# Performance work log

Hardware: AMD Instinct MI355X
Metric: run time of the kernel (lower is better)

Reference implementation:

```python
import jax, jax.numpy as jnp
import numpy as np
from jax.scipy.special import gammaln

NSTEP, NGRID, MU, LENF = 730, 1500, 16, 15
PRECS = 1e-5

# [low, high] physical ranges for the 12 HBV parameters (same order as torch code)
PARA_SCALE = np.array([[1, 6], [50, 1000], [0.05, 0.9], [0.01, 0.5], [0.001, 0.2],
                       [0.2, 1], [0, 10], [0, 100], [-2.5, 2.5], [0.5, 10],
                       [0, 0.1], [0, 0.2]], dtype=np.float32)
ROUT_SCALE = np.array([[0, 2.9], [0, 6.5]], dtype=np.float32)


def setup_inputs() -> dict:
    key = jax.random.key(0)
    kp, kt, ke, kpar, krt = jax.random.split(key, 5)
    P = jax.random.uniform(kp, (NSTEP, NGRID), jnp.float32) * 10.0   # precip mm/day
    T = jax.random.normal(kt, (NSTEP, NGRID), jnp.float32) * 8.0     # temp degC
    ETp = jax.random.uniform(ke, (NSTEP, NGRID), jnp.float32) * 5.0  # PET mm/day
    x = jnp.stack([P, T, ETp], axis=-1)                              # [Nstep, Ngrid, 3]
    parameters = jax.random.uniform(kpar, (NGRID, 12, MU), jnp.float32)
    rtwts = jax.random.uniform(krt, (NGRID, 2), jnp.float32)
    return {"x": x, "parameters": parameters, "rtwts": rtwts, "mu": MU}


def _hbv(x, parameters, rtwts, mu):
    Nstep, Ngrid = x.shape[0], x.shape[1]
    # scale raw [0,1] parameters into physical ranges; each is [Ngrid, mu]
    lo, hi = PARA_SCALE[:, 0], PARA_SCALE[:, 1]
    par = [lo[i] + parameters[:, i, :] * (hi[i] - lo[i]) for i in range(12)]
    (parBETA, parFC, parK0, parK1, parK2, parLP, parPERC, parUZL,
     parTT, parCFMAX, parCFR, parCWH) = par

    P, T, ETp = x[:, :, 0], x[:, :, 1], x[:, :, 2]  # each [Nstep, Ngrid]

    init = tuple(jnp.full((Ngrid, mu), 0.001, jnp.float32) for _ in range(5))

    def step(carry, inp):
        SNOWPACK, MELTWATER, SM, SUZ, SLZ = carry
        Pt, Tt, Et = inp
        Pm, Tm, ETpm = Pt[:, None], Tt[:, None], Et[:, None]  # [Ngrid, 1]
        is_rain = (Tm >= parTT).astype(jnp.float32)
        RAIN = Pm * is_rain
        SNOW = Pm * (1.0 - is_rain)
        SNOWPACK = SNOWPACK + SNOW
        melt = jnp.minimum(jnp.maximum(parCFMAX * (Tm - parTT), 0.0), SNOWPACK)
        MELTWATER = MELTWATER + melt
        SNOWPACK = SNOWPACK - melt
        refreezing = jnp.minimum(jnp.maximum(parCFR * parCFMAX * (parTT - Tm), 0.0), MELTWATER)
        SNOWPACK = SNOWPACK + refreezing
        MELTWATER = MELTWATER - refreezing
        tosoil = jnp.maximum(MELTWATER - parCWH * SNOWPACK, 0.0)
        MELTWATER = MELTWATER - tosoil
        soil_wetness = jnp.clip((SM / parFC) ** parBETA, 0.0, 1.0)
        recharge = (RAIN + tosoil) * soil_wetness
        SM = SM + RAIN + tosoil - recharge
        excess = jnp.maximum(SM - parFC, 0.0)
        SM = SM - excess
        evapfactor = jnp.clip(SM / (parLP * parFC), 0.0, 1.0)
        ETact = jnp.minimum(SM, ETpm * evapfactor)
        SM = jnp.maximum(SM - ETact, PRECS)
        SUZ = SUZ + recharge + excess
        PERC = jnp.minimum(SUZ, parPERC)
        SUZ = SUZ - PERC
        Q0 = parK0 * jnp.maximum(SUZ - parUZL, 0.0)
        SUZ = SUZ - Q0
        Q1 = parK1 * SUZ
        SUZ = SUZ - Q1
        SLZ = SLZ + PERC
        Q2 = parK2 * SLZ
        SLZ = SLZ - Q2
        return (SNOWPACK, MELTWATER, SM, SUZ, SLZ), (Q0 + Q1 + Q2, Q0, Q1, Q2, ETact)

    _, (Qsimmu, Q0s, Q1s, Q2s, ETmu) = jax.lax.scan(step, init, (P, T, ETp))

    Qsimave = Qsimmu.mean(-1)  # [Nstep, Ngrid]  (muwts is None)

    # gamma unit hydrograph routing (routOpt=True, comprout=False)
    tempa = ROUT_SCALE[0, 0] + rtwts[:, 0] * (ROUT_SCALE[0, 1] - ROUT_SCALE[0, 0])
    tempb = ROUT_SCALE[1, 0] + rtwts[:, 1] * (ROUT_SCALE[1, 1] - ROUT_SCALE[1, 0])
    aa = jnp.maximum(tempa, 0.0) + 0.1      # [Ngrid]
    theta = jnp.maximum(tempb, 0.0) + 0.5   # [Ngrid]
    t = jnp.arange(LENF, dtype=jnp.float32) + 0.5  # [lenF]
    # w[k, g] = t_k^(a-1) * exp(-t_k/theta) / (Gamma(a) * theta^a)
    w = (jnp.exp(-gammaln(aa))[None, :] * theta[None, :] ** (-aa[None, :])
         * t[:, None] ** (aa[None, :] - 1.0) * jnp.exp(-t[:, None] / theta[None, :]))
    w = w / w.sum(0)  # normalize over kernel axis -> [lenF, Ngrid]

    # causal depthwise conv over time: Qs[n,g] = sum_k w[k,g] * Qsimave[n-k,g]
    xpad = jnp.pad(Qsimave, ((LENF - 1, 0), (0, 0)))
    Qs = jnp.zeros_like(Qsimave)
    for k in range(LENF):
        Qs = Qs + w[k][None, :] * jax.lax.dynamic_slice_in_dim(xpad, LENF - 1 - k, Nstep, 0)
    Qs = Qs[..., None]  # [Nstep, Ngrid, 1]

    Qall = jnp.concatenate([Qs,
                            Q0s.mean(-1, keepdims=True),
                            Q1s.mean(-1, keepdims=True),
                            Q2s.mean(-1, keepdims=True),
                            ETmu.mean(-1, keepdims=True)], axis=-1)
    return Qall  # [Nstep, Ngrid, 5]


def reference(x, parameters, rtwts, mu):
    return _hbv(x, parameters, rtwts, mu)
```

## Files before the change

### kernel.cpp

```cpp
#include <hip/hip_runtime.h>
#include <math.h>

#define NSTEP  730
#define NGRID  1500
#define LENF   15
#define PRECS  1e-5f
#define CH     16
#define NCHUNK 46
#define NPHASE (NCHUNK+3)
#define QROW   260
#define OTW    21

static __device__ __forceinline__ float fexp2(float v){ return __builtin_amdgcn_exp2f(v); }
static __device__ __forceinline__ float flog2(float v){ return __builtin_amdgcn_logf(v); }

#define PIPE_BARRIER() do { \
    asm volatile("s_waitcnt lgkmcnt(0)" ::: "memory"); \
    __builtin_amdgcn_sched_barrier(0); \
    __builtin_amdgcn_s_barrier(); \
    __builtin_amdgcn_sched_barrier(0); \
} while(0)

__global__ __launch_bounds__(256, 1)
void hbv_scan_kernel(const float* __restrict__ x,
                     const float* __restrict__ params,
                     const float* __restrict__ rtwts,
                     float* __restrict__ out)
{
    __shared__ float  xring[3*CH*16];
    __shared__ float  rtbuf[2*CH*64];
    __shared__ float2 soilbuf[2*CH*64];
    __shared__ float  qbuf[2*CH*QROW];
    __shared__ float  outtile[CH*OTW];
    __shared__ float  ring[4*64];

    const int tid  = threadIdx.x;
    const int wid  = tid >> 6;
    const int lane = tid & 63;
    const int gl = lane >> 4, m = lane & 15;
    const int b  = blockIdx.x;
    const int g  = b*4 + gl;
    const float inv16 = 1.f/16.f;

    if (wid == 3) {
        #pragma unroll
        for (int j = 0; j < 3; ++j) {
            const int idx = lane + 64*j;
            const int r = idx/12, rem = idx - 12*r;
            const int gi = rem/3, ch = rem - 3*gi;
            xring[r*16 + gi*4 + ch] = x[r*4500 + b*12 + gi*3 + ch];
        }
    }
    ring[tid & 255] = 0.f;
    PIPE_BARRIER();

    if (wid == 0) {
        const float pTT     = -2.5f + params[(g*12+8)*16+m]*5.f;
        const float pCFMAX  =  0.5f + params[(g*12+9)*16+m]*9.5f;
        const float refCoef = (params[(g*12+10)*16+m]*0.1f)*pCFMAX;
        const float pCWH    =          params[(g*12+11)*16+m]*0.2f;
        const float negCMTT = -pCFMAX*pTT;
        const float refCTT  = refCoef*pTT;
        float SP = 0.001f, MW = 0.001f;
        for (int p = 0; p < NPHASE; ++p) {
            if (p < NCHUNK) {
                const float* xb = &xring[(p%3)*CH*16 + gl*4];
                float* rb = &rtbuf[(p&1)*CH*64 + lane];
                float2 PT[CH];
                #pragma unroll
                for (int s = 0; s < CH; ++s)
                    PT[s] = *(const float2*)(xb + s*16);
                #pragma unroll
                for (int s = 0; s < CH; ++s) {
                    const float Pm = PT[s].x, Tm = PT[s].y;
                    const float RAIN    = (Tm >= pTT) ? Pm : 0.f;
                    const float meltcap = fmaxf(fmaf(pCFMAX, Tm, negCMTT), 0.f);
                    const float refcap  = fmaxf(fmaf(-refCoef, Tm, refCTT), 0.f);
                    const float SP1 = SP + (Pm - RAIN);
                    const float melt = fminf(meltcap, SP1);
                    const float MW1 = MW + melt;
                    const float refreeze = fminf(refcap, MW1);
                    SP = SP1 - melt + refreeze;
                    const float MW2 = MW1 - refreeze;
                    const float tosoil = fmaxf(fmaf(-pCWH, SP, MW2), 0.f);
                    MW = MW2 - tosoil;
                    rb[s*64] = RAIN + tosoil;
                }
            }
            PIPE_BARRIER();
        }
    } else if (wid == 1) {
        const float bb  = 1.f  + params[(g*12+0)*16+m]*5.f;
        const float pFC = 50.f + params[(g*12+1)*16+m]*950.f;
        const float pLP = 0.2f + params[(g*12+5)*16+m]*0.8f;
        const float iLPFC = 1.f/(pLP*pFC);
        const float cc = -bb * flog2(pFC);
        float SM = 0.001f;
        for (int p = 0; p < NPHASE; ++p) {
            if (p >= 1 && p-1 < NCHUNK) {
                const int c = p-1;
                const float* xe = &xring[(c%3)*CH*16 + gl*4 + 2];
                const float* rb = &rtbuf[(c&1)*CH*64 + lane];
                float2* sb = &soilbuf[(c&1)*CH*64 + lane];
                float rt[CH], Ev[CH];
                #pragma unroll
                for (int s = 0; s < CH; ++s) { rt[s] = rb[s*64]; Ev[s] = xe[s*16]; }
                #pragma unroll
                for (int s = 0; s < CH; ++s) {
                    const float sw  = fexp2(fmaf(bb, flog2(SM), cc));
                    const float SM1 = fmaf(-rt[s], sw, SM + rt[s]);
                    const float SM2 = fminf(SM1, pFC);
                    const float cE  = Ev[s] * iLPFC;
                    const float et  = fminf(fminf(SM2*cE, SM2), Ev[s]);
                    const float re  = fmaf(rt[s], sw, SM1 - SM2);
                    SM = fmaxf(fmaxf(fmaf(-SM2, cE, SM2), SM2 - Ev[s]), PRECS);
                    sb[s*64] = make_float2(re, et);
                }
            }
            PIPE_BARRIER();
        }
    } else if (wid == 2) {
        const float pK0   = 0.05f  + params[(g*12+2)*16+m]*0.85f;
        const float pK1   = 0.01f  + params[(g*12+3)*16+m]*0.49f;
        const float pK2   = 0.001f + params[(g*12+4)*16+m]*0.199f;
        const float pPERC =          params[(g*12+6)*16+m]*10.f;
        const float pUZL  =          params[(g*12+7)*16+m]*100.f;
        const float oneMinusK0 = 1.f - pK0, K0UZL = pK0*pUZL;
        float SUZ = 0.001f, SLZ = 0.001f;
        for (int p = 0; p < NPHASE; ++p) {
            if (p >= 2 && p-2 < NCHUNK) {
                const int c = p-2;
                const float2* sb = &soilbuf[(c&1)*CH*64 + lane];
                float* qb = &qbuf[(c&1)*CH*QROW + lane*4];
                float2 rE[CH];
                #pragma unroll
                for (int s = 0; s < CH; ++s) rE[s] = sb[s*64];
                #pragma unroll
                for (int s = 0; s < CH; ++s) {
                    const float SUZ1 = SUZ + rE[s].x;
                    const float SUZ2 = fmaxf(SUZ1 - pPERC, 0.f);
                    const float PERC = SUZ1 - SUZ2;
                    const float SUZ3 = fminf(SUZ2, fmaf(SUZ2, oneMinusK0, K0UZL));
                    const float Q0 = SUZ2 - SUZ3;
                    const float Q1 = pK1 * SUZ3;
                    SUZ = SUZ3 - Q1;
                    const float SLZ1 = SLZ + PERC;
                    const float Q2 = pK2 * SLZ1;
                    SLZ = SLZ1 - Q2;
                    *(float4*)(qb + s*QROW) = make_float4(Q0, Q1, Q2, rE[s].y);
                }
            }
            PIPE_BARRIER();
        }
    } else {
        float wq[LENF];
        {
            const float ta  = rtwts[g*2+0] * 2.9f;
            const float tbv = rtwts[g*2+1] * 6.5f;
            const float aa = fmaxf(ta, 0.f) + 0.1f;
            const float th = fmaxf(tbv, 0.f) + 0.5f;
            const float c0v = expf(-lgammaf(aa)) * powf(th, -aa);
            float wsum = 0.f;
            #pragma unroll
            for (int k = 0; k < LENF; ++k) {
                const float tt = (float)k + 0.5f;
                wq[k] = c0v * powf(tt, aa-1.f) * expf(-tt/th);
                wsum += wq[k];
            }
            const float ws = inv16 / wsum;
            #pragma unroll
            for (int k = 0; k < LENF; ++k) wq[k] *= ws;
        }
        int rbase[3], bcol[3], lslot[3];
        #pragma unroll
        for (int j = 0; j < 3; ++j) {
            const int idx = lane + 64*j;
            const int r = idx/12, rem = idx - 12*r;
            const int gi = rem/3, ch = rem - 3*gi;
            rbase[j] = r;
            bcol[j]  = b*12 + gi*3 + ch;
            lslot[j] = r*16 + gi*4 + ch;
        }
        int st_o[5], st_g[5];
        #pragma unroll
        for (int j = 0; j < 5; ++j) {
            const int idx = lane + 64*j;
            const int tt = idx/20, cl = idx - 20*tt;
            st_o[j] = tt*OTW + cl;
            st_g[j] = tt*7500 + cl;
        }

        for (int p = 0; p < NPHASE; ++p) {
            const bool do_stage = (p+1 < NCHUNK);
            float stg0=0.f, stg1=0.f, stg2=0.f;
            if (do_stage) {
                int r0 = (p+1)*CH + rbase[0]; r0 = (r0 < NSTEP) ? r0 : (NSTEP-1);
                int r1 = (p+1)*CH + rbase[1]; r1 = (r1 < NSTEP) ? r1 : (NSTEP-1);
                int r2 = (p+1)*CH + rbase[2]; r2 = (r2 < NSTEP) ? r2 : (NSTEP-1);
                stg0 = x[r0*4500 + bcol[0]];
                stg1 = x[r1*4500 + bcol[1]];
                stg2 = x[r2*4500 + bcol[2]];
            }
            const int q = p - 3;
            if (q >= 0) {
                const int nstep = (q == NCHUNK-1) ? (NSTEP - (NCHUNK-1)*CH) : CH;
                const float* qb = &qbuf[(q&1)*CH*QROW];
                const int t = q*CH + m;
                float a0=0.f, a1=0.f, a2=0.f, a3=0.f;
                if (m < nstep) {
                    float4 v[16];
                    #pragma unroll
                    for (int i = 0; i < 16; ++i)
                        v[i] = *(const float4*)&qb[m*QROW + gl*64 + i*4];
                    float4 s0 = v[0], s1 = v[1], s2 = v[2], s3 = v[3];
                    #pragma unroll
                    for (int i = 4; i < 16; i += 4) {
                        s0.x+=v[i].x;   s0.y+=v[i].y;   s0.z+=v[i].z;   s0.w+=v[i].w;
                        s1.x+=v[i+1].x; s1.y+=v[i+1].y; s1.z+=v[i+1].z; s1.w+=v[i+1].w;
                        s2.x+=v[i+2].x; s2.y+=v[i+2].y; s2.z+=v[i+2].z; s2.w+=v[i+2].w;
                        s3.x+=v[i+3].x; s3.y+=v[i+3].y; s3.z+=v[i+3].z; s3.w+=v[i+3].w;
                    }
                    a0 = (s0.x+s1.x) + (s2.x+s3.x);
                    a1 = (s0.y+s1.y) + (s2.y+s3.y);
                    a2 = (s0.z+s1.z) + (s2.z+s3.z);
                    a3 = (s0.w+s1.w) + (s2.w+s3.w);
                    ring[gl*64 + (t & 63)] = a0 + a1 + a2;
                }
                asm volatile("s_waitcnt lgkmcnt(0)" ::: "memory");
                if (m < nstep) {
                    float rv[LENF];
                    #pragma unroll
                    for (int k = 0; k < LENF; ++k)
                        rv[k] = ring[gl*64 + ((t - k) & 63)];
                    float accA = 0.f, accB = 0.f;
                    #pragma unroll
                    for (int k = 0; k < LENF-1; k += 2) {
                        accA = fmaf(wq[k],   rv[k],   accA);
                        accB = fmaf(wq[k+1], rv[k+1], accB);
                    }
                    accA = fmaf(wq[LENF-1], rv[LENF-1], accA);
                    float* ot = &outtile[m*OTW + gl*5];
                    ot[0] = accA + accB;
                    ot[1] = a0*inv16; ot[2] = a1*inv16;
                    ot[3] = a2*inv16; ot[4] = a3*inv16;
                }
                asm volatile("s_waitcnt lgkmcnt(0)" ::: "memory");
                const int ndw = nstep*20;
                float* ob = out + q*CH*7500 + b*20;
                #pragma unroll
                for (int j = 0; j < 5; ++j) {
                    const int idx = lane + 64*j;
                    if (idx < ndw) ob[st_g[j]] = outtile[st_o[j]];
                }
            }
            if (do_stage) {
                float* xd = &xring[((p+1)%3)*CH*16];
                xd[lslot[0]] = stg0; xd[lslot[1]] = stg1; xd[lslot[2]] = stg2;
            }
            PIPE_BARRIER();
        }
    }
}

extern "C" void kernel_launch(void* const* d_in, const int* in_sizes, int n_in,
                              void* d_out, int out_size, void* d_ws, size_t ws_size,
                              hipStream_t stream)
{
    const float* x      = (const float*)d_in[0];
    const float* params = (const float*)d_in[1];
    const float* rt     = (const float*)d_in[2];
    float* out = (float*)d_out;

    dim3 grid(NGRID / 4), block(256);
    hipLaunchKernelGGL(hbv_scan_kernel, grid, block, 0, stream, x, params, rt, out);
}
```

Before: 60.53 us.

## Pack two independent HBV pipelines into each 512-thread block

Each block now runs two copies of the four-wave producer/consumer pipeline, one per half of a 512-thread block, covering 8 grid cells instead of 4. Every LDS buffer is duplicated per pipe, and out-of-range grid cells in the last block are clamped on reads and masked on stores. The intent is to halve the block count and change how the work spreads across CUs. The cost is that one block-wide barrier now couples both pipes, so each phase waits for the slower of the two.

```diff
diff --git a/kernel.cpp b/kernel.cpp
--- a/kernel.cpp
+++ b/kernel.cpp
@@ -21,26 +21,35 @@
     __builtin_amdgcn_sched_barrier(0); \
 } while(0)
 
-__global__ __launch_bounds__(256, 1)
+__global__ __launch_bounds__(512, 1)
 void hbv_scan_kernel(const float* __restrict__ x,
                      const float* __restrict__ params,
                      const float* __restrict__ rtwts,
                      float* __restrict__ out)
 {
-    __shared__ float  xring[3*CH*16];
-    __shared__ float  rtbuf[2*CH*64];
-    __shared__ float2 soilbuf[2*CH*64];
-    __shared__ float  qbuf[2*CH*QROW];
-    __shared__ float  outtile[CH*OTW];
-    __shared__ float  ring[4*64];
+    __shared__ float  xringA[2][3*CH*16];
+    __shared__ float  rtbufA[2][2*CH*64];
+    __shared__ float2 soilA [2][2*CH*64];
+    __shared__ float  qbufA [2][2*CH*QROW];
+    __shared__ float  outtA [2][CH*OTW];
+    __shared__ float  ringA [2][4*64];
 
     const int tid  = threadIdx.x;
-    const int wid  = tid >> 6;
+    const int pipe = tid >> 8;
+    const int wid  = (tid >> 6) & 3;
     const int lane = tid & 63;
     const int gl = lane >> 4, m = lane & 15;
     const int b  = blockIdx.x;
-    const int g  = b*4 + gl;
+    const int g  = b*8 + pipe*4 + gl;
+    const int gc = (g < NGRID) ? g : (NGRID-1);
     const float inv16 = 1.f/16.f;
+
+    float*  xring   = xringA[pipe];
+    float*  rtbuf   = rtbufA[pipe];
+    float2* soilbuf = soilA[pipe];
+    float*  qbuf    = qbufA[pipe];
+    float*  outtile = outtA[pipe];
+    float*  ring    = ringA[pipe];
 
     if (wid == 3) {
         #pragma unroll
@@ -48,17 +57,19 @@
             const int idx = lane + 64*j;
             const int r = idx/12, rem = idx - 12*r;
             const int gi = rem/3, ch = rem - 3*gi;
-            xring[r*16 + gi*4 + ch] = x[r*4500 + b*12 + gi*3 + ch];
+            int col = b*24 + pipe*12 + gi*3 + ch;
+            if (col >= 4500) col = 4497 + ch;
+            xring[r*16 + gi*4 + ch] = x[r*4500 + col];
         }
     }
     ring[tid & 255] = 0.f;
     PIPE_BARRIER();
 
     if (wid == 0) {
-        const float pTT     = -2.5f + params[(g*12+8)*16+m]*5.f;
-        const float pCFMAX  =  0.5f + params[(g*12+9)*16+m]*9.5f;
-        const float refCoef = (params[(g*12+10)*16+m]*0.1f)*pCFMAX;
-        const float pCWH    =          params[(g*12+11)*16+m]*0.2f;
+        const float pTT     = -2.5f + params[(gc*12+8)*16+m]*5.f;
+        const float pCFMAX  =  0.5f + params[(gc*12+9)*16+m]*9.5f;
+        const float refCoef = (params[(gc*12+10)*16+m]*0.1f)*pCFMAX;
+        const float pCWH    =          params[(gc*12+11)*16+m]*0.2f;
         const float negCMTT = -pCFMAX*pTT;
         const float refCTT  = refCoef*pTT;
         float SP = 0.001f, MW = 0.001f;
@@ -90,9 +101,9 @@
             PIPE_BARRIER();
         }
     } else if (wid == 1) {
-        const float bb  = 1.f  + params[(g*12+0)*16+m]*5.f;
-        const float pFC = 50.f + params[(g*12+1)*16+m]*950.f;
-        const float pLP = 0.2f + params[(g*12+5)*16+m]*0.8f;
+        const float bb  = 1.f  + params[(gc*12+0)*16+m]*5.f;
+        const float pFC = 50.f + params[(gc*12+1)*16+m]*950.f;
+        const float pLP = 0.2f + params[(gc*12+5)*16+m]*0.8f;
         const float iLPFC = 1.f/(pLP*pFC);
         const float cc = -bb * flog2(pFC);
         float SM = 0.001f;
@@ -120,11 +131,11 @@
             PIPE_BARRIER();
         }
     } else if (wid == 2) {
-        const float pK0   = 0.05f  + params[(g*12+2)*16+m]*0.85f;
-        const float pK1   = 0.01f  + params[(g*12+3)*16+m]*0.49f;
-        const float pK2   = 0.001f + params[(g*12+4)*16+m]*0.199f;
-        const float pPERC =          params[(g*12+6)*16+m]*10.f;
-        const float pUZL  =          params[(g*12+7)*16+m]*100.f;
+        const float pK0   = 0.05f  + params[(gc*12+2)*16+m]*0.85f;
+        const float pK1   = 0.01f  + params[(gc*12+3)*16+m]*0.49f;
+        const float pK2   = 0.001f + params[(gc*12+4)*16+m]*0.199f;
+        const float pPERC =          params[(gc*12+6)*16+m]*10.f;
+        const float pUZL  =          params[(gc*12+7)*16+m]*100.f;
         const float oneMinusK0 = 1.f - pK0, K0UZL = pK0*pUZL;
         float SUZ = 0.001f, SLZ = 0.001f;
         for (int p = 0; p < NPHASE; ++p) {
@@ -155,8 +166,8 @@
     } else {
         float wq[LENF];
         {
-            const float ta  = rtwts[g*2+0] * 2.9f;
-            const float tbv = rtwts[g*2+1] * 6.5f;
+            const float ta  = rtwts[gc*2+0] * 2.9f;
+            const float tbv = rtwts[gc*2+1] * 6.5f;
             const float aa = fmaxf(ta, 0.f) + 0.1f;
             const float th = fmaxf(tbv, 0.f) + 0.5f;
             const float c0v = expf(-lgammaf(aa)) * powf(th, -aa);
@@ -178,16 +189,19 @@
             const int r = idx/12, rem = idx - 12*r;
             const int gi = rem/3, ch = rem - 3*gi;
             rbase[j] = r;
-            bcol[j]  = b*12 + gi*3 + ch;
+            int col = b*24 + pipe*12 + gi*3 + ch;
+            if (col >= 4500) col = 4497 + ch;
+            bcol[j]  = col;
             lslot[j] = r*16 + gi*4 + ch;
         }
-        int st_o[5], st_g[5];
+        int st_o[5], st_g[5], st_ok[5];
         #pragma unroll
         for (int j = 0; j < 5; ++j) {
             const int idx = lane + 64*j;
             const int tt = idx/20, cl = idx - 20*tt;
             st_o[j] = tt*OTW + cl;
             st_g[j] = tt*7500 + cl;
+            st_ok[j] = (b*40 + pipe*20 + cl < 7500);
         }
 
         for (int p = 0; p < NPHASE; ++p) {
@@ -246,11 +260,11 @@
                 }
                 asm volatile("s_waitcnt lgkmcnt(0)" ::: "memory");
                 const int ndw = nstep*20;
-                float* ob = out + q*CH*7500 + b*20;
+                float* ob = out + q*CH*7500 + b*40 + pipe*20;
                 #pragma unroll
                 for (int j = 0; j < 5; ++j) {
                     const int idx = lane + 64*j;
-                    if (idx < ndw) ob[st_g[j]] = outtile[st_o[j]];
+                    if (idx < ndw && st_ok[j]) ob[st_g[j]] = outtile[st_o[j]];
                 }
             }
             if (do_stage) {
@@ -271,6 +285,6 @@
     const float* rt     = (const float*)d_in[2];
     float* out = (float*)d_out;
 
-    dim3 grid(NGRID / 4), block(256);
+    dim3 grid((NGRID + 7) / 8), block(512);
     hipLaunchKernelGGL(hbv_scan_kernel, grid, block, 0, stream, x, params, rt, out);
 }
```

Result: slower. 70.60 us (+16.6%).
